# Performance work log

Hardware: AMD Instinct MI355X
Metric: run time of the kernel (lower is better)

Reference implementation:

```python
import jax, jax.numpy as jnp
import numpy as np

N = 65536      # flattened tokens
K = 8192       # codebook_size
D = 64         # codebook_dim
DECAY = 0.9
EPS = 1e-05


def setup_inputs() -> dict:
    key = jax.random.key(0)
    k1, k2, k3, k4 = jax.random.split(key, 4)
    z = jax.random.normal(k1, (N, D), dtype=jnp.float32)
    # codebook initialized uniform(-1, 1) in the torch module
    weight = jax.random.uniform(k2, (K, D), dtype=jnp.float32, minval=-1.0, maxval=1.0)
    # EMA state: positive cluster sizes, embed_avg near the codebook
    cluster_size = jax.random.uniform(k3, (K,), dtype=jnp.float32)
    embed_avg = weight + 0.01 * jax.random.normal(k4, (K, D), dtype=jnp.float32)
    return {"z": z, "weight": weight, "cluster_size": cluster_size, "embed_avg": embed_avg}


def reference(z, weight, cluster_size, embed_avg):
    # VectorQuantizer.ema_update: distances -> argmin -> gather -> EMA stats -> weight refresh
    zd = jax.lax.stop_gradient(z)  # torch uses z.detach() for distance/quant_error
    # distance[n,k] = ||z_n||^2 + ||c_k||^2 - 2 z_n . c_k   (addmm pattern)
    dist = (zd * zd).sum(1, keepdims=True) + (weight * weight).sum(1) - 2.0 * (zd @ weight.T)  # [N, K]
    token = jnp.argmin(dist, axis=1)                      # [N]
    embed = weight[token]                                  # gather [N, D]
    quant_error = jnp.mean(((embed - zd) ** 2).sum(1))

    # onehot_probs.sum(0) == per-code counts; onehot.T @ z == segment sum of z
    counts = jax.ops.segment_sum(jnp.ones((zd.shape[0],), zd.dtype), token, num_segments=K)  # [K]
    embed_sum = jax.ops.segment_sum(z, token, num_segments=K)                                # [K, D]

    new_cluster_size = cluster_size * DECAY + (1.0 - DECAY) * counts
    new_embed_avg = embed_avg * DECAY + (1.0 - DECAY) * embed_sum

    # ema_weight_update with num_tokens = codebook_size
    n = new_cluster_size.sum()
    smoothed = (new_cluster_size + EPS) / (n + K * EPS) * n
    new_weight = new_embed_avg / smoothed[:, None]

    return quant_error, new_weight, new_cluster_size, new_embed_avg
```

## Files before the change

kernel.cpp:

```cpp
#include <hip/hip_runtime.h>
#include <type_traits>

#define N_TOK 65536
#define K_CODE 8192
#define D_DIM 64

constexpr float DECAY = 0.9f;
constexpr float OMD = 0.1f;
constexpr float EPS = 1e-5f;

constexpr int OUT_QE = 0;
constexpr int OUT_W  = 1;
constexpr int OUT_CS = 1 + K_CODE * D_DIM;
constexpr int OUT_EA = OUT_CS + K_CODE;

constexpr int WS_QE     = 0;
constexpr int WS_NSUM   = 1;
constexpr int WS_COUNTS = 16;
constexpr int WS_EMBSUM = WS_COUNTS + K_CODE;
constexpr int WS_WHI    = WS_EMBSUM + K_CODE * D_DIM;
constexpr int WS_WLO    = WS_WHI + K_CODE * D_DIM / 2;
constexpr int WS_CNP    = WS_WLO + K_CODE * D_DIM / 2;
constexpr int WS_ZERO   = WS_WHI;

typedef __attribute__((ext_vector_type(16))) float floatx16;
typedef __attribute__((ext_vector_type(8)))  short short8;
typedef __attribute__((ext_vector_type(8)))  __bf16 bf16x8;

template <typename T, typename = void> struct mfma_takes : std::false_type {};
template <typename T>
struct mfma_takes<T, std::void_t<decltype(__builtin_amdgcn_mfma_f32_32x32x16_bf16(
    std::declval<T>(), std::declval<T>(), std::declval<floatx16>(), 0, 0, 0))>>
    : std::true_type {};

__device__ __forceinline__ floatx16 MFMA(short8 a, short8 b, floatx16 c) {
  if constexpr (mfma_takes<bf16x8>::value) {
    return __builtin_amdgcn_mfma_f32_32x32x16_bf16(
        __builtin_bit_cast(bf16x8, a), __builtin_bit_cast(bf16x8, b), c, 0, 0, 0);
  } else {
    return __builtin_amdgcn_mfma_f32_32x32x16_bf16(a, b, c, 0, 0, 0);
  }
}

__device__ __forceinline__ unsigned short bf16rne(float x) {
  unsigned int u = __float_as_uint(x);
  return (unsigned short)((u + 0x7FFFu + ((u >> 16) & 1u)) >> 16);
}

__device__ __forceinline__ void gload_lds16(const unsigned short* g, unsigned short* l) {
#if defined(__has_builtin) && __has_builtin(__builtin_amdgcn_global_load_lds)
  typedef __attribute__((address_space(1))) void gvoid;
  typedef __attribute__((address_space(3))) void lvoid;
  __builtin_amdgcn_global_load_lds((gvoid*)g, (lvoid*)l, 16, 0, 0);
#else
  *(uint4*)l = *(const uint4*)g;
#endif
}
__device__ __forceinline__ void gload_lds4(const unsigned int* g, unsigned int* l) {
#if defined(__has_builtin) && __has_builtin(__builtin_amdgcn_global_load_lds)
  typedef __attribute__((address_space(1))) void gvoid;
  typedef __attribute__((address_space(3))) void lvoid;
  __builtin_amdgcn_global_load_lds((gvoid*)g, (lvoid*)l, 4, 0, 0);
#else
  *l = *g;
#endif
}

__global__ void vq_prep(const float* __restrict__ w, float* __restrict__ ws) {
  const int tid = threadIdx.x;
  const int d = tid & 63;
  const int k = blockIdx.x * 4 + (tid >> 6);
  const float v = w[(size_t)k * D_DIM + d];
  const unsigned short h = bf16rne(v);
  const float hf = __uint_as_float((unsigned int)h << 16);
  const unsigned short l = bf16rne(v - hf);
  unsigned short* whi = (unsigned short*)(ws + WS_WHI);
  unsigned short* wlo = (unsigned short*)(ws + WS_WLO);
  const int pos = k * D_DIM + (((d >> 3) ^ (k & 7)) * 8) + (d & 7);
  whi[pos] = h;
  wlo[pos] = l;
  float s = v * v;
#pragma unroll
  for (int m = 32; m >= 1; m >>= 1) s += __shfl_xor(s, m);
  if (d == 0) {
    const float cn64 = s + 64.0f;
    const unsigned short ch = bf16rne(cn64);
    const float chf = __uint_as_float((unsigned int)ch << 16);
    const unsigned short cl = bf16rne(cn64 - chf);
    ((unsigned int*)(ws + WS_CNP))[k] = (unsigned int)ch | ((unsigned int)cl << 16);
  }
}

__global__ __launch_bounds__(256, 2) void vq_argmin(
    const float* __restrict__ z, float* __restrict__ ws)
{
  __shared__ __align__(16) unsigned short Wbuf[4][2][2][32 * 64];
  __shared__ unsigned int Wcn[4][2][64];
  __shared__ float mind_s[2][128];
  __shared__ int   tok_s[2][128];

  const int tid  = threadIdx.x;
  const int w    = tid >> 6;
  const int lane = tid & 63;
  const int m    = lane & 31;
  const int h    = lane >> 5;
  const int hw   = w & 1;
  const int tg   = w >> 1;
  const int tb   = blockIdx.x * 128;

  const unsigned short* whiP = (const unsigned short*)(ws + WS_WHI) + (size_t)hw * 4096 * D_DIM;
  const unsigned short* wloP = (const unsigned short*)(ws + WS_WLO) + (size_t)hw * 4096 * D_DIM;
  const unsigned int*   cnpP = (const unsigned int*)(ws + WS_CNP) + hw * 4096;

  auto issueStage = [&](int s, int b) {
    const size_t roff = (size_t)s * (32 * D_DIM) + lane * 8;
#pragma unroll
    for (int i = 0; i < 4; ++i)
      gload_lds16(whiP + roff + i * 512, &Wbuf[w][b][0][i * 512]);
#pragma unroll
    for (int i = 0; i < 4; ++i)
      gload_lds16(wloP + roff + i * 512, &Wbuf[w][b][1][i * 512]);
    gload_lds4(cnpP + s * 32 + lane, &Wcn[w][b][0]);
  };

  issueStage(0, 0);

  short8 ah[2][4], al[2][4];
  float znorm[2];
#pragma unroll
  for (int set = 0; set < 2; ++set) {
    const float* zrow = z + (size_t)(tb + tg * 64 + set * 32 + m) * D_DIM + 8 * h;
    float zn = 0.f;
#pragma unroll
    for (int s4 = 0; s4 < 4; ++s4) {
      const float4 v0 = *(const float4*)(zrow + 16 * s4);
      const float4 v1 = *(const float4*)(zrow + 16 * s4 + 4);
      const float vals[8] = {v0.x, v0.y, v0.z, v0.w, v1.x, v1.y, v1.z, v1.w};
#pragma unroll
      for (int j = 0; j < 8; ++j) {
        const float x = vals[j];
        zn += x * x;
        const float y = -2.0f * x;
        const unsigned short hb = bf16rne(y);
        const float hf = __uint_as_float((unsigned int)hb << 16);
        const unsigned short lb = bf16rne(y - hf);
        ah[set][s4][j] = (short)hb;
        al[set][s4][j] = (short)lb;
      }
    }
    zn += __shfl_xor(zn, 32);
    znorm[set] = zn;
  }

  short8 acn;
  {
    uint4 ab = {0u, 0u, 0u, 0u};
    ab.x = (h == 0) ? 0x3F803F80u : 0u;
    acn = __builtin_bit_cast(short8, ab);
  }

  float kmin[2][16];
#pragma unroll
  for (int set = 0; set < 2; ++set)
#pragma unroll
    for (int r = 0; r < 16; ++r) kmin[set][r] = 3.4e38f;

  int xoff[4];
#pragma unroll
  for (int s4 = 0; s4 < 4; ++s4) xoff[s4] = ((2 * s4 + h) ^ (m & 7)) * 8;
  const int mrow = m * 64;
  const floatx16 kZero = {};

  for (int s = 0; s < 128; ++s) {
    const int b = s & 1;
    asm volatile("s_waitcnt lgkmcnt(0)" ::: "memory");
    issueStage((s + 1) & 127, b ^ 1);
    asm volatile("s_waitcnt vmcnt(9)" ::: "memory");

    short8 bh[4], bl[4];
#pragma unroll
    for (int s4 = 0; s4 < 4; ++s4) {
      bh[s4] = *(const short8*)&Wbuf[w][b][0][mrow + xoff[s4]];
      bl[s4] = *(const short8*)&Wbuf[w][b][1][mrow + xoff[s4]];
    }
    short8 bcn;
    {
      uint4 bb = {0u, 0u, 0u, 0u};
      bb.x = (h == 0) ? Wcn[w][b][m] : 0u;
      bcn = __builtin_bit_cast(short8, bb);
    }

    const floatx16 head = MFMA(acn, bcn, kZero);
    floatx16 a0, a1;
    a0 = MFMA(ah[0][0], bh[0], head);
    a1 = MFMA(ah[1][0], bh[0], head);
#pragma unroll
    for (int s4 = 1; s4 < 4; ++s4) {
      a0 = MFMA(ah[0][s4], bh[s4], a0);
      a1 = MFMA(ah[1][s4], bh[s4], a1);
    }
#pragma unroll
    for (int s4 = 0; s4 < 4; ++s4) {
      a0 = MFMA(al[0][s4], bh[s4], a0);
      a1 = MFMA(al[1][s4], bh[s4], a1);
    }
#pragma unroll
    for (int s4 = 0; s4 < 4; ++s4) {
      a0 = MFMA(ah[0][s4], bl[s4], a0);
      a1 = MFMA(ah[1][s4], bl[s4], a1);
    }

#pragma unroll
    for (int r = 0; r < 16; ++r) {
      kmin[0][r] = fminf(kmin[0][r],
          __uint_as_float((__float_as_uint(a0[r]) & 0xFFFFFF00u) | (unsigned)s));
      kmin[1][r] = fminf(kmin[1][r],
          __uint_as_float((__float_as_uint(a1[r]) & 0xFFFFFF00u) | (unsigned)s));
    }
  }

#pragma unroll
  for (int set = 0; set < 2; ++set) {
#pragma unroll
    for (int r = 0; r < 16; ++r) {
      float kv = kmin[set][r];
      int mo = m;
#pragma unroll
      for (int mm = 1; mm < 32; mm <<= 1) {
        const float ov = __shfl_xor(kv, mm);
        const int   om = __shfl_xor(mo, mm);
        if (ov < kv || (ov == kv && om < mo)) { kv = ov; mo = om; }
      }
      const int mr = (r & 3) + 8 * (r >> 2) + 4 * h;
      if (m == mr) {
        const unsigned int kb = __float_as_uint(kv);
        const int t = tg * 64 + set * 32 + mr;
        tok_s[hw][t] = hw * 4096 + (int)(kb & 0xFFu) * 32 + mo;
        mind_s[hw][t] = __uint_as_float(kb & 0xFFFFFF00u) - 64.0f + znorm[set];
      }
    }
  }
  __syncthreads();

  float* counts = ws + WS_COUNTS;
  float* embsum = ws + WS_EMBSUM;

  if (tid < 128) {
    const float d0 = mind_s[0][tid], d1 = mind_s[1][tid];
    const int   i0 = tok_s[0][tid],  i1 = tok_s[1][tid];
    const bool t1 = d1 < d0;
    const float dm = t1 ? d1 : d0;
    const int   im = t1 ? i1 : i0;
    tok_s[0][tid] = im;
    float qe = dm;
#pragma unroll
    for (int mm = 32; mm >= 1; mm >>= 1) qe += __shfl_xor(qe, mm);
    if ((tid & 63) == 0) atomicAdd(ws + WS_QE, qe);
    atomicAdd(&counts[im], 1.0f);
  }
  __syncthreads();

#pragma unroll 4
  for (int t = 0; t < 32; ++t) {
    const int row = w * 32 + t;
    const int tk = tok_s[0][row];
    const float zv = z[(size_t)(tb + row) * D_DIM + lane];
    atomicAdd(&embsum[(size_t)tk * D_DIM + lane], zv);
  }
}

__global__ void vq_finalize_cs(const float* __restrict__ cluster_size,
                               float* __restrict__ ws, float* __restrict__ out)
{
  const int k = blockIdx.x * 256 + threadIdx.x;
  const float ncs = cluster_size[k] * DECAY + OMD * ws[WS_COUNTS + k];
  out[OUT_CS + k] = ncs;
  float s = ncs;
#pragma unroll
  for (int m = 32; m >= 1; m >>= 1) s += __shfl_xor(s, m);
  __shared__ float part[4];
  if ((threadIdx.x & 63) == 0) part[threadIdx.x >> 6] = s;
  __syncthreads();
  if (threadIdx.x == 0) {
    atomicAdd(ws + WS_NSUM, part[0] + part[1] + part[2] + part[3]);
    if (blockIdx.x == 0) out[OUT_QE] = ws[WS_QE] * (1.0f / N_TOK);
  }
}

__global__ void vq_finalize_w(const float* __restrict__ embed_avg,
                              const float* __restrict__ ws, float* __restrict__ out)
{
  const int idx = blockIdx.x * 256 + threadIdx.x;
  const int k = idx >> 6;
  const float nea = embed_avg[idx] * DECAY + OMD * ws[WS_EMBSUM + idx];
  out[OUT_EA + idx] = nea;
  const float n = ws[WS_NSUM];
  const float ncs = out[OUT_CS + k];
  const float sm = (ncs + EPS) / (n + K_CODE * EPS) * n;
  out[OUT_W + idx] = nea / sm;
}

extern "C" void kernel_launch(void* const* d_in, const int* in_sizes, int n_in,
                              void* d_out, int out_size, void* d_ws, size_t ws_size,
                              hipStream_t stream) {
  const float* z  = (const float*)d_in[0];
  const float* w  = (const float*)d_in[1];
  const float* cs = (const float*)d_in[2];
  const float* ea = (const float*)d_in[3];
  float* out = (float*)d_out;
  float* ws  = (float*)d_ws;

  (void)hipMemsetAsync(d_ws, 0, (size_t)WS_ZERO * sizeof(float), stream);

  vq_prep<<<K_CODE / 4, 256, 0, stream>>>(w, ws);
  vq_argmin<<<N_TOK / 128, 256, 0, stream>>>(z, ws);
  vq_finalize_cs<<<K_CODE / 256, 256, 0, stream>>>(cs, ws, out);
  vq_finalize_w<<<K_CODE * D_DIM / 256, 256, 0, stream>>>(ea, ws, out);
}
```

Before: 320.7 us.

## Load codebook fragments directly to registers from pre-packed layout, drop LDS staging

```diff
diff --git a/kernel.cpp b/kernel.cpp
--- a/kernel.cpp
+++ b/kernel.cpp
@@ -18,10 +18,9 @@
 constexpr int WS_NSUM   = 1;
 constexpr int WS_COUNTS = 16;
 constexpr int WS_EMBSUM = WS_COUNTS + K_CODE;
-constexpr int WS_WHI    = WS_EMBSUM + K_CODE * D_DIM;
-constexpr int WS_WLO    = WS_WHI + K_CODE * D_DIM / 2;
-constexpr int WS_CNP    = WS_WLO + K_CODE * D_DIM / 2;
-constexpr int WS_ZERO   = WS_WHI;
+constexpr int WS_WPK    = WS_EMBSUM + K_CODE * D_DIM;
+constexpr int WS_CNP    = WS_WPK + (2 * K_CODE * D_DIM + 8192) / 2;
+constexpr int WS_ZERO   = WS_WPK;
 
 typedef __attribute__((ext_vector_type(16))) float floatx16;
 typedef __attribute__((ext_vector_type(8)))  short short8;
@@ -47,41 +46,23 @@
   return (unsigned short)((u + 0x7FFFu + ((u >> 16) & 1u)) >> 16);
 }
 
-__device__ __forceinline__ void gload_lds16(const unsigned short* g, unsigned short* l) {
-#if defined(__has_builtin) && __has_builtin(__builtin_amdgcn_global_load_lds)
-  typedef __attribute__((address_space(1))) void gvoid;
-  typedef __attribute__((address_space(3))) void lvoid;
-  __builtin_amdgcn_global_load_lds((gvoid*)g, (lvoid*)l, 16, 0, 0);
-#else
-  *(uint4*)l = *(const uint4*)g;
-#endif
-}
-__device__ __forceinline__ void gload_lds4(const unsigned int* g, unsigned int* l) {
-#if defined(__has_builtin) && __has_builtin(__builtin_amdgcn_global_load_lds)
-  typedef __attribute__((address_space(1))) void gvoid;
-  typedef __attribute__((address_space(3))) void lvoid;
-  __builtin_amdgcn_global_load_lds((gvoid*)g, (lvoid*)l, 4, 0, 0);
-#else
-  *l = *g;
-#endif
-}
-
 __global__ void vq_prep(const float* __restrict__ w, float* __restrict__ ws) {
   const int tid = threadIdx.x;
   const int d = tid & 63;
   const int k = blockIdx.x * 4 + (tid >> 6);
   const float v = w[(size_t)k * D_DIM + d];
-  const unsigned short h = bf16rne(v);
-  const float hf = __uint_as_float((unsigned int)h << 16);
-  const unsigned short l = bf16rne(v - hf);
-  unsigned short* whi = (unsigned short*)(ws + WS_WHI);
-  unsigned short* wlo = (unsigned short*)(ws + WS_WLO);
-  const int pos = k * D_DIM + (((d >> 3) ^ (k & 7)) * 8) + (d & 7);
-  whi[pos] = h;
-  wlo[pos] = l;
+  const unsigned short hbits = bf16rne(v);
+  const float hf = __uint_as_float((unsigned int)hbits << 16);
+  const unsigned short lbits = bf16rne(v - hf);
+  unsigned short* wp = (unsigned short*)(ws + WS_WPK);
+  const int c = k >> 5, m = k & 31;
+  const int s4 = d >> 4, hh = (d >> 3) & 1, j = d & 7;
+  const int lanepos = (hh * 32 + m) * 8 + j;
+  wp[(size_t)(c * 8 + s4) * 512 + lanepos]     = hbits;
+  wp[(size_t)(c * 8 + 4 + s4) * 512 + lanepos] = lbits;
   float s = v * v;
 #pragma unroll
-  for (int m = 32; m >= 1; m >>= 1) s += __shfl_xor(s, m);
+  for (int mm = 32; mm >= 1; mm >>= 1) s += __shfl_xor(s, mm);
   if (d == 0) {
     const float cn64 = s + 64.0f;
     const unsigned short ch = bf16rne(cn64);
@@ -91,45 +72,27 @@
   }
 }
 
-__global__ __launch_bounds__(256, 2) void vq_argmin(
+__global__ __launch_bounds__(256, 3) void vq_argmin(
     const float* __restrict__ z, float* __restrict__ ws)
 {
-  __shared__ __align__(16) unsigned short Wbuf[4][2][2][32 * 64];
-  __shared__ unsigned int Wcn[4][2][64];
-  __shared__ float mind_s[2][128];
-  __shared__ int   tok_s[2][128];
+  __shared__ float mind_s[4][64];
+  __shared__ int   tok_s[4][64];
 
   const int tid  = threadIdx.x;
-  const int w    = tid >> 6;
+  const int cq   = tid >> 6;
   const int lane = tid & 63;
   const int m    = lane & 31;
   const int h    = lane >> 5;
-  const int hw   = w & 1;
-  const int tg   = w >> 1;
-  const int tb   = blockIdx.x * 128;
-
-  const unsigned short* whiP = (const unsigned short*)(ws + WS_WHI) + (size_t)hw * 4096 * D_DIM;
-  const unsigned short* wloP = (const unsigned short*)(ws + WS_WLO) + (size_t)hw * 4096 * D_DIM;
-  const unsigned int*   cnpP = (const unsigned int*)(ws + WS_CNP) + hw * 4096;
-
-  auto issueStage = [&](int s, int b) {
-    const size_t roff = (size_t)s * (32 * D_DIM) + lane * 8;
-#pragma unroll
-    for (int i = 0; i < 4; ++i)
-      gload_lds16(whiP + roff + i * 512, &Wbuf[w][b][0][i * 512]);
-#pragma unroll
-    for (int i = 0; i < 4; ++i)
-      gload_lds16(wloP + roff + i * 512, &Wbuf[w][b][1][i * 512]);
-    gload_lds4(cnpP + s * 32 + lane, &Wcn[w][b][0]);
-  };
-
-  issueStage(0, 0);
+  const int tb   = blockIdx.x * 64;
+
+  const unsigned short* wp = (const unsigned short*)(ws + WS_WPK);
+  const unsigned int* cnp = (const unsigned int*)(ws + WS_CNP);
 
   short8 ah[2][4], al[2][4];
   float znorm[2];
 #pragma unroll
   for (int set = 0; set < 2; ++set) {
-    const float* zrow = z + (size_t)(tb + tg * 64 + set * 32 + m) * D_DIM + 8 * h;
+    const float* zrow = z + (size_t)(tb + set * 32 + m) * D_DIM + 8 * h;
     float zn = 0.f;
 #pragma unroll
     for (int s4 = 0; s4 < 4; ++s4) {
@@ -165,49 +128,47 @@
 #pragma unroll
     for (int r = 0; r < 16; ++r) kmin[set][r] = 3.4e38f;
 
-  int xoff[4];
-#pragma unroll
-  for (int s4 = 0; s4 < 4; ++s4) xoff[s4] = ((2 * s4 + h) ^ (m & 7)) * 8;
-  const int mrow = m * 64;
+  const unsigned short* wlane = wp + lane * 8;
+  auto LD = [&](int slot) -> short8 {
+    return *(const short8*)(wlane + (size_t)slot * 512);
+  };
+
+  const int c0 = cq * 64;
+  short8 bufh[2], bufl[2];
+  bufh[0] = LD(c0 * 8 + 0); bufl[0] = LD(c0 * 8 + 4);
+  bufh[1] = LD(c0 * 8 + 1); bufl[1] = LD(c0 * 8 + 5);
+  unsigned int cnq = cnp[cq * 2048 + m];
+
   const floatx16 kZero = {};
 
-  for (int s = 0; s < 128; ++s) {
-    const int b = s & 1;
-    asm volatile("s_waitcnt lgkmcnt(0)" ::: "memory");
-    issueStage((s + 1) & 127, b ^ 1);
-    asm volatile("s_waitcnt vmcnt(9)" ::: "memory");
-
-    short8 bh[4], bl[4];
-#pragma unroll
-    for (int s4 = 0; s4 < 4; ++s4) {
-      bh[s4] = *(const short8*)&Wbuf[w][b][0][mrow + xoff[s4]];
-      bl[s4] = *(const short8*)&Wbuf[w][b][1][mrow + xoff[s4]];
-    }
+  for (int s = 0; s < 64; ++s) {
+    const int cslot = (c0 + s) * 8;
+    const unsigned int cn_cur = cnq;
+    cnq = cnp[cq * 2048 + (s + 1) * 32 + m];
+
     short8 bcn;
     {
       uint4 bb = {0u, 0u, 0u, 0u};
-      bb.x = (h == 0) ? Wcn[w][b][m] : 0u;
+      bb.x = (h == 0) ? cn_cur : 0u;
       bcn = __builtin_bit_cast(short8, bb);
     }
-
     const floatx16 head = MFMA(acn, bcn, kZero);
-    floatx16 a0, a1;
-    a0 = MFMA(ah[0][0], bh[0], head);
-    a1 = MFMA(ah[1][0], bh[0], head);
-#pragma unroll
-    for (int s4 = 1; s4 < 4; ++s4) {
-      a0 = MFMA(ah[0][s4], bh[s4], a0);
-      a1 = MFMA(ah[1][s4], bh[s4], a1);
-    }
+    floatx16 a0 = head, a1 = head;
+
 #pragma unroll
     for (int s4 = 0; s4 < 4; ++s4) {
-      a0 = MFMA(al[0][s4], bh[s4], a0);
-      a1 = MFMA(al[1][s4], bh[s4], a1);
-    }
-#pragma unroll
-    for (int s4 = 0; s4 < 4; ++s4) {
-      a0 = MFMA(ah[0][s4], bl[s4], a0);
-      a1 = MFMA(ah[1][s4], bl[s4], a1);
+      const int p = s4 & 1;
+      const short8 bh = bufh[p];
+      const short8 bl = bufl[p];
+      const int nslot = cslot + s4 + 2 + ((s4 >> 1) * 4);
+      bufh[p] = LD(nslot);
+      bufl[p] = LD(nslot + 4);
+      a0 = MFMA(ah[0][s4], bh, a0);
+      a1 = MFMA(ah[1][s4], bh, a1);
+      a0 = MFMA(al[0][s4], bh, a0);
+      a1 = MFMA(al[1][s4], bh, a1);
+      a0 = MFMA(ah[0][s4], bl, a0);
+      a1 = MFMA(ah[1][s4], bl, a1);
     }
 
 #pragma unroll
@@ -234,9 +195,9 @@
       const int mr = (r & 3) + 8 * (r >> 2) + 4 * h;
       if (m == mr) {
         const unsigned int kb = __float_as_uint(kv);
-        const int t = tg * 64 + set * 32 + mr;
-        tok_s[hw][t] = hw * 4096 + (int)(kb & 0xFFu) * 32 + mo;
-        mind_s[hw][t] = __uint_as_float(kb & 0xFFFFFF00u) - 64.0f + znorm[set];
+        const int t = set * 32 + mr;
+        tok_s[cq][t] = cq * 2048 + (int)(kb & 0xFFu) * 32 + mo;
+        mind_s[cq][t] = __uint_as_float(kb & 0xFFFFFF00u) - 64.0f + znorm[set];
       }
     }
   }
@@ -245,24 +206,27 @@
   float* counts = ws + WS_COUNTS;
   float* embsum = ws + WS_EMBSUM;
 
-  if (tid < 128) {
-    const float d0 = mind_s[0][tid], d1 = mind_s[1][tid];
-    const int   i0 = tok_s[0][tid],  i1 = tok_s[1][tid];
-    const bool t1 = d1 < d0;
-    const float dm = t1 ? d1 : d0;
-    const int   im = t1 ? i1 : i0;
+  if (tid < 64) {
+    float dm = mind_s[0][tid];
+    int   im = tok_s[0][tid];
+#pragma unroll
+    for (int q = 1; q < 4; ++q) {
+      const float dq = mind_s[q][tid];
+      const int   iq = tok_s[q][tid];
+      if (dq < dm) { dm = dq; im = iq; }
+    }
     tok_s[0][tid] = im;
     float qe = dm;
 #pragma unroll
     for (int mm = 32; mm >= 1; mm >>= 1) qe += __shfl_xor(qe, mm);
-    if ((tid & 63) == 0) atomicAdd(ws + WS_QE, qe);
+    if (tid == 0) atomicAdd(ws + WS_QE, qe);
     atomicAdd(&counts[im], 1.0f);
   }
   __syncthreads();
 
 #pragma unroll 4
-  for (int t = 0; t < 32; ++t) {
-    const int row = w * 32 + t;
+  for (int t = 0; t < 16; ++t) {
+    const int row = cq * 16 + t;
     const int tk = tok_s[0][row];
     const float zv = z[(size_t)(tb + row) * D_DIM + lane];
     atomicAdd(&embsum[(size_t)tk * D_DIM + lane], zv);
@@ -313,7 +277,7 @@
   (void)hipMemsetAsync(d_ws, 0, (size_t)WS_ZERO * sizeof(float), stream);
 
   vq_prep<<<K_CODE / 4, 256, 0, stream>>>(w, ws);
-  vq_argmin<<<N_TOK / 128, 256, 0, stream>>>(z, ws);
+  vq_argmin<<<N_TOK / 64, 256, 0, stream>>>(z, ws);
   vq_finalize_cs<<<K_CODE / 256, 256, 0, stream>>>(cs, ws, out);
   vq_finalize_w<<<K_CODE * D_DIM / 256, 256, 0, stream>>>(ea, ws, out);
 }
```

Result: faster. 303.2 us (-5.5%).
